# Kernel optimization log

Measured on AMD Instinct MI355X. Metric: run time of the kernel, lower is better.

The kernel has to match this reference:

```python
import jax, jax.numpy as jnp
import numpy as np

EMB = 1024
HEADS = 16
HEAD_DIM = EMB // HEADS
FF = 4 * EMB
EPS = 1e-5


def setup_inputs() -> dict:
    key = jax.random.key(0)
    ks = jax.random.split(key, 16)
    s = 0.02
    return {
        "x": jax.random.normal(ks[0], (2, 2048, EMB), dtype=jnp.float32),
        "ln1_g": jnp.ones((EMB,), jnp.float32),
        "ln1_b": jnp.zeros((EMB,), jnp.float32),
        "Wq": jax.random.normal(ks[1], (EMB, EMB), jnp.float32) * s,
        "bq": jnp.zeros((EMB,), jnp.float32),
        "Wk": jax.random.normal(ks[2], (EMB, EMB), jnp.float32) * s,
        "bk": jnp.zeros((EMB,), jnp.float32),
        "Wv": jax.random.normal(ks[3], (EMB, EMB), jnp.float32) * s,
        "bv": jnp.zeros((EMB,), jnp.float32),
        "Wo": jax.random.normal(ks[4], (EMB, EMB), jnp.float32) * s,
        "bo": jnp.zeros((EMB,), jnp.float32),
        "ln2_g": jnp.ones((EMB,), jnp.float32),
        "ln2_b": jnp.zeros((EMB,), jnp.float32),
        "W1": jax.random.normal(ks[5], (EMB, FF), jnp.float32) * s,
        "b1": jnp.zeros((FF,), jnp.float32),
        "W2": jax.random.normal(ks[6], (FF, EMB), jnp.float32) * s,
        "b2": jnp.zeros((EMB,), jnp.float32),
    }


def _layernorm(x, g, b):
    mu = jnp.mean(x, axis=-1, keepdims=True)
    var = jnp.var(x, axis=-1, keepdims=True)
    return (x - mu) * jax.lax.rsqrt(var + EPS) * g + b


def _attention(x, Wq, bq, Wk, bk, Wv, bv, Wo, bo):
    B, T, C = x.shape
    # [B,T,C] -> [B,H,T,Dh]
    def split(y):
        return y.reshape(B, T, HEADS, HEAD_DIM).transpose(0, 2, 1, 3)
    Q = split(x @ Wq + bq)
    K = split(x @ Wk + bk)
    V = split(x @ Wv + bv)
    att = jnp.einsum("bhqd,bhkd->bhqk", Q, K) / np.sqrt(HEAD_DIM).astype(np.float32)
    causal = jnp.tril(jnp.ones((T, T), bool))
    att = jnp.where(causal, att, -jnp.inf)
    att = jax.nn.softmax(att, axis=-1)
    out = jnp.einsum("bhqk,bhkd->bhqd", att, V)
    out = out.transpose(0, 2, 1, 3).reshape(B, T, C)
    return out @ Wo + bo


def reference(x, ln1_g, ln1_b, Wq, bq, Wk, bk, Wv, bv, Wo, bo,
              ln2_g, ln2_b, W1, b1, W2, b2):
    # dropout is identity in eval mode
    x = x + _attention(_layernorm(x, ln1_g, ln1_b), Wq, bq, Wk, bk, Wv, bv, Wo, bo)
    h = _layernorm(x, ln2_g, ln2_b)
    h = jax.nn.gelu(h @ W1 + b1, approximate=False) @ W2 + b2
    return x + h
```

## Files before the change

### kernel.cpp

```cpp
#include <hip/hip_runtime.h>
#include <hip/hip_bf16.h>

typedef __attribute__((ext_vector_type(4))) float f32x4;
typedef __attribute__((ext_vector_type(8))) short bf16x8;
typedef unsigned int u32;
typedef unsigned short u16;

#define GASP __attribute__((address_space(1)))
#define LASP __attribute__((address_space(3)))

__device__ __forceinline__ u16 f2bf(float f) {
  u32 u = __float_as_uint(f);
  return (u16)((u + 0x7fffu + ((u >> 16) & 1u)) >> 16);
}

__device__ __forceinline__ u32 cvtpk(float lo, float hi) {
  u32 r;
  asm("v_cvt_pk_bf16_f32 %0, %1, %2" : "=v"(r) : "v"(lo), "v"(hi));
  return r;
}

__device__ __forceinline__ void gl_lds16(const void* g, void* l) {
  __builtin_amdgcn_global_load_lds((const GASP u32*)g, (LASP u32*)l, 16, 0, 0);
}

struct CastArgs {
  const float* s[6];
  u16* d[6];
};

__global__ __launch_bounds__(256) void cast_w(CastArgs a) {
  int bid = blockIdx.x;
  int w, t, K, N, kshift;
  if (bid < 4096)      { w = bid >> 10; t = bid & 1023; K = 1024; N = 1024; kshift = 5; }
  else if (bid < 8192) { w = 4; t = bid - 4096; K = 1024; N = 4096; kshift = 5; }
  else                 { w = 5; t = bid - 8192; K = 4096; N = 1024; kshift = 7; }
  int tk = t & ((1 << kshift) - 1);
  int tn = t >> kshift;
  int k0 = tk << 5, n0 = tn << 5;
  const float* src = a.s[w];
  u16* dst = a.d[w];
  __shared__ u16 tile[32][36];
  int r = threadIdx.x >> 3, c0 = (threadIdx.x & 7) << 2;
  float4 v = *(const float4*)&src[(size_t)(k0 + r) * N + n0 + c0];
  tile[c0 + 0][r] = f2bf(v.x);
  tile[c0 + 1][r] = f2bf(v.y);
  tile[c0 + 2][r] = f2bf(v.z);
  tile[c0 + 3][r] = f2bf(v.w);
  __syncthreads();
  ushort4 o;
  o.x = tile[r][c0 + 0];
  o.y = tile[r][c0 + 1];
  o.z = tile[r][c0 + 2];
  o.w = tile[r][c0 + 3];
  *(ushort4*)&dst[(size_t)(n0 + r) * K + k0 + c0] = o;
}

__global__ __launch_bounds__(256) void ln_k(const float* __restrict__ x, const float* __restrict__ g,
                                            const float* __restrict__ b, u16* __restrict__ out) {
  int row = blockIdx.x;
  int tid = threadIdx.x;
  float4 v = *(const float4*)&x[(size_t)row * 1024 + tid * 4];
  float s = v.x + v.y + v.z + v.w;
  float ss = v.x * v.x + v.y * v.y + v.z * v.z + v.w * v.w;
#pragma unroll
  for (int o = 32; o >= 1; o >>= 1) {
    s += __shfl_xor(s, o, 64);
    ss += __shfl_xor(ss, o, 64);
  }
  __shared__ float red[8];
  int wv = tid >> 6;
  if ((tid & 63) == 0) { red[wv] = s; red[wv + 4] = ss; }
  __syncthreads();
  s = red[0] + red[1] + red[2] + red[3];
  ss = red[4] + red[5] + red[6] + red[7];
  float mu = s * (1.0f / 1024.0f);
  float var = ss * (1.0f / 1024.0f) - mu * mu;
  float rstd = rsqrtf(var + 1e-5f);
  float4 gv = *(const float4*)&g[tid * 4];
  float4 bv = *(const float4*)&b[tid * 4];
  ushort4 o4;
  o4.x = f2bf((v.x - mu) * rstd * gv.x + bv.x);
  o4.y = f2bf((v.y - mu) * rstd * gv.y + bv.y);
  o4.z = f2bf((v.z - mu) * rstd * gv.z + bv.z);
  o4.w = f2bf((v.w - mu) * rstd * gv.w + bv.w);
  *(ushort4*)&out[(size_t)row * 1024 + tid * 4] = o4;
}

template <int MODE>
__global__ __launch_bounds__(512, 2) void gemm_256(
    const u16* __restrict__ A, const u16* __restrict__ Bt,
    const float* __restrict__ bias0, const float* __restrict__ bias1, const float* __restrict__ bias2,
    void* outp, int rm, int rn, int xn, int M, int N, int K) {
  __shared__ __align__(16) u16 As[4][128 * 64];
  __shared__ __align__(16) u16 Bs[4][128 * 64];
  char* asB = (char*)As;
  char* bsB = (char*)Bs;
  const int tid = threadIdx.x;
  const int w = tid >> 6, lane = tid & 63;
  const int xcd = blockIdx.x & 7, idx = blockIdx.x >> 3;
  const int mt = (xcd / xn) * rm + (idx % rm);
  const int nt = (xcd % xn) * rn + (idx / rm);
  const int m0 = mt << 8, n0 = nt << 8;

  const int rA = tid >> 3;
  const int csw = ((tid & 7) ^ (rA & 7)) * 8;
  const u16* pA = A + (size_t)(m0 + rA) * K + csw;
  const u16* pB = Bt + (size_t)(n0 + rA) * K + csw;
  const int dstOff = tid * 16;

#define STG_A(kt, h, d_) do {                                            \
    const u16* s_ = pA + (size_t)((h) * 128) * K + (size_t)(kt) * 64;    \
    char* l_ = asB + ((d_) * 2 + (h)) * 16384 + dstOff;                  \
    gl_lds16(s_, l_);                                                    \
    gl_lds16(s_ + (size_t)64 * K, l_ + 8192);                            \
  } while (0)
#define STG_B(kt, h, d_) do {                                            \
    const u16* s_ = pB + (size_t)((h) * 128) * K + (size_t)(kt) * 64;    \
    char* l_ = bsB + ((d_) * 2 + (h)) * 16384 + dstOff;                  \
    gl_lds16(s_, l_);                                                    \
    gl_lds16(s_ + (size_t)64 * K, l_ + 8192);                            \
  } while (0)

  const int wr = w >> 2, wc = w & 3;
  const int g = lane >> 4, qi = lane & 15;

  int aOff[8][2], bOff[4][2];
#pragma unroll
  for (int mm = 0; mm < 8; ++mm) {
    int row = mm * 16 + qi;
#pragma unroll
    for (int ks = 0; ks < 2; ++ks)
      aOff[mm][ks] = row * 128 + (((ks * 4 + g) ^ (qi & 7)) << 4);
  }
#pragma unroll
  for (int nn = 0; nn < 4; ++nn) {
    int rowb = (wc & 1) * 64 + nn * 16 + qi;
#pragma unroll
    for (int ks = 0; ks < 2; ++ks)
      bOff[nn][ks] = rowb * 128 + (((ks * 4 + g) ^ (qi & 7)) << 4);
  }

  f32x4 acc[8][4];
#pragma unroll
  for (int i = 0; i < 8; ++i)
#pragma unroll
    for (int j = 0; j < 4; ++j) acc[i][j] = f32x4{0.f, 0.f, 0.f, 0.f};

#define MFMA16(MB, A00, A01, A10, A11) do {                                              \
    __builtin_amdgcn_s_setprio(1);                                                       \
    acc[(MB)][0] = __builtin_amdgcn_mfma_f32_16x16x32_bf16(A00, bv[0][0], acc[(MB)][0], 0, 0, 0); \
    acc[(MB)][1] = __builtin_amdgcn_mfma_f32_16x16x32_bf16(A00, bv[1][0], acc[(MB)][1], 0, 0, 0); \
    acc[(MB)][2] = __builtin_amdgcn_mfma_f32_16x16x32_bf16(A00, bv[2][0], acc[(MB)][2], 0, 0, 0); \
    acc[(MB)][3] = __builtin_amdgcn_mfma_f32_16x16x32_bf16(A00, bv[3][0], acc[(MB)][3], 0, 0, 0); \
    acc[(MB) + 1][0] = __builtin_amdgcn_mfma_f32_16x16x32_bf16(A10, bv[0][0], acc[(MB) + 1][0], 0, 0, 0); \
    acc[(MB) + 1][1] = __builtin_amdgcn_mfma_f32_16x16x32_bf16(A10, bv[1][0], acc[(MB) + 1][1], 0, 0, 0); \
    acc[(MB) + 1][2] = __builtin_amdgcn_mfma_f32_16x16x32_bf16(A10, bv[2][0], acc[(MB) + 1][2], 0, 0, 0); \
    acc[(MB) + 1][3] = __builtin_amdgcn_mfma_f32_16x16x32_bf16(A10, bv[3][0], acc[(MB) + 1][3], 0, 0, 0); \
    acc[(MB)][0] = __builtin_amdgcn_mfma_f32_16x16x32_bf16(A01, bv[0][1], acc[(MB)][0], 0, 0, 0); \
    acc[(MB)][1] = __builtin_amdgcn_mfma_f32_16x16x32_bf16(A01, bv[1][1], acc[(MB)][1], 0, 0, 0); \
    acc[(MB)][2] = __builtin_amdgcn_mfma_f32_16x16x32_bf16(A01, bv[2][1], acc[(MB)][2], 0, 0, 0); \
    acc[(MB)][3] = __builtin_amdgcn_mfma_f32_16x16x32_bf16(A01, bv[3][1], acc[(MB)][3], 0, 0, 0); \
    acc[(MB) + 1][0] = __builtin_amdgcn_mfma_f32_16x16x32_bf16(A11, bv[0][1], acc[(MB) + 1][0], 0, 0, 0); \
    acc[(MB) + 1][1] = __builtin_amdgcn_mfma_f32_16x16x32_bf16(A11, bv[1][1], acc[(MB) + 1][1], 0, 0, 0); \
    acc[(MB) + 1][2] = __builtin_amdgcn_mfma_f32_16x16x32_bf16(A11, bv[2][1], acc[(MB) + 1][2], 0, 0, 0); \
    acc[(MB) + 1][3] = __builtin_amdgcn_mfma_f32_16x16x32_bf16(A11, bv[3][1], acc[(MB) + 1][3], 0, 0, 0); \
    __builtin_amdgcn_s_setprio(0);                                                       \
  } while (0)

#define RDA(dst0, dst1, MB)                                          \
    bf16x8 dst0##0 = *(const bf16x8*)(asB + aTB + aOff[(MB)][0]);     \
    bf16x8 dst0##1 = *(const bf16x8*)(asB + aTB + aOff[(MB)][1]);     \
    bf16x8 dst1##0 = *(const bf16x8*)(asB + aTB + aOff[(MB) + 1][0]); \
    bf16x8 dst1##1 = *(const bf16x8*)(asB + aTB + aOff[(MB) + 1][1]);

  const int T = K >> 6;
  STG_A(0, 0, 0); STG_A(0, 1, 0);
  STG_B(0, 0, 0); STG_B(0, 1, 0);
  if (T > 1) {
    STG_B(1, 0, 1); STG_B(1, 1, 1);
    asm volatile("s_waitcnt vmcnt(4)" ::: "memory");
  } else {
    asm volatile("s_waitcnt vmcnt(0)" ::: "memory");
  }
  __builtin_amdgcn_s_barrier();

  for (int t = 0; t < T; ++t) {
    const int d = t & 1;
    const int aTB = (d * 2 + wr) * 16384;
    const int bTB = (d * 2 + (wc >> 1)) * 16384;
    bf16x8 bv[4][2];
#pragma unroll
    for (int nn = 0; nn < 4; ++nn) {
      bv[nn][0] = *(const bf16x8*)(bsB + bTB + bOff[nn][0]);
      bv[nn][1] = *(const bf16x8*)(bsB + bTB + bOff[nn][1]);
    }
    RDA(p0a, p0b, 0);
    asm volatile("" ::: "memory");
    if (t + 1 < T) STG_A(t + 1, 0, d ^ 1);
    __builtin_amdgcn_s_barrier();
    MFMA16(0, p0a0, p0a1, p0b0, p0b1);
    __builtin_amdgcn_s_barrier();
    {
      RDA(p1a, p1b, 2);
      asm volatile("" ::: "memory");
      if (t + 1 < T) STG_A(t + 1, 1, d ^ 1);
      __builtin_amdgcn_s_barrier();
      MFMA16(2, p1a0, p1a1, p1b0, p1b1);
      __builtin_amdgcn_s_barrier();
    }
    {
      RDA(p2a, p2b, 4);
      asm volatile("" ::: "memory");
      if (t + 2 < T) STG_B(t + 2, 0, d);
      __builtin_amdgcn_s_barrier();
      MFMA16(4, p2a0, p2a1, p2b0, p2b1);
      __builtin_amdgcn_s_barrier();
    }
    {
      RDA(p3a, p3b, 6);
      asm volatile("" ::: "memory");
      if (t + 2 < T) STG_B(t + 2, 1, d);
      __builtin_amdgcn_s_barrier();
      MFMA16(6, p3a0, p3a1, p3b0, p3b1);
      if (t < T - 2)       { asm volatile("s_waitcnt vmcnt(4)" ::: "memory"); }
      else if (t == T - 2) { asm volatile("s_waitcnt vmcnt(0)" ::: "memory"); }
      __builtin_amdgcn_s_barrier();
    }
  }
#undef MFMA16
#undef RDA
#undef STG_A
#undef STG_B

  const int ci = lane & 15;
#pragma unroll
  for (int mm = 0; mm < 8; ++mm) {
#pragma unroll
    for (int nn = 0; nn < 4; ++nn) {
      int colb = n0 + wc * 64 + nn * 16 + ci;
      int rowbase = m0 + wr * 128 + mm * 16 + 4 * g;
      f32x4 c = acc[mm][nn];
      if constexpr (MODE == 2) {
        int sel = colb >> 10;
        int cc = colb & 1023;
        const float* bp = sel == 0 ? bias0 : (sel == 1 ? bias1 : bias2);
        float bb = bp[cc];
        int h = cc >> 6, dd = cc & 63;
        int b_ = rowbase >> 11, tt = rowbase & 2047;
        if (sel == 2) {
          u16* op = (u16*)outp + 2ull * (4096ull * 1024ull);
          ushort4 o4;
          o4.x = f2bf(c[0] + bb);
          o4.y = f2bf(c[1] + bb);
          o4.z = f2bf(c[2] + bb);
          o4.w = f2bf(c[3] + bb);
          *(ushort4*)&op[((size_t)(b_ * 16 + h) * 64 + dd) * 2048 + tt] = o4;
        } else {
          float scale = (sel == 0) ? 0.125f : 1.0f;
          u16* op = (u16*)outp + (size_t)sel * (4096ull * 1024ull);
#pragma unroll
          for (int r = 0; r < 4; ++r)
            op[((size_t)(b_ * 16 + h) * 2048 + tt + r) * 64 + dd] = f2bf((c[r] + bb) * scale);
        }
      } else {
        float bb = bias0[colb];
#pragma unroll
        for (int r = 0; r < 4; ++r) {
          float v = c[r] + bb;
          float gl = 0.5f * v * (1.0f + erff(v * 0.70710678118654752f));
          ((u16*)outp)[(size_t)(rowbase + r) * N + colb] = f2bf(gl);
        }
      }
    }
  }
}

__global__ __launch_bounds__(512) void gemm_sk(
    const u16* __restrict__ A, const u16* __restrict__ Bt,
    const float* __restrict__ bias0, float* __restrict__ outp,
    const float* __restrict__ res, int M, int N, int K) {
  __shared__ __align__(16) union SM {
    struct { u16 As[2][4][128 * 32]; u16 Bs[2][4][128 * 32]; } t;
    float red[16][4][4][64];
  } sm;
  const int tid = threadIdx.x;
  const int w8 = tid >> 6, lane = tid & 63;
  const int gg = w8 >> 2, wl = w8 & 3;
  const int m0 = blockIdx.y << 7, n0 = blockIdx.x << 7;

  char* asB = (char*)sm.t.As[gg];
  char* bsB = (char*)sm.t.Bs[gg];
  const u16* aS[2];
  const u16* bS[2];
#pragma unroll
  for (int i = 0; i < 2; ++i) {
    int p = wl * 2048 + i * 1024 + lane * 16;
    int r = p >> 6;
    int cl = ((p >> 4) & 3) ^ ((r >> 1) & 3);
    aS[i] = A + (size_t)(m0 + r) * K + gg * 32 + cl * 8;
    bS[i] = Bt + (size_t)(n0 + r) * K + gg * 32 + cl * 8;
  }
  f32x4 acc[4][4];
#pragma unroll
  for (int i = 0; i < 4; ++i)
#pragma unroll
    for (int j = 0; j < 4; ++j) acc[i][j] = f32x4{0.f, 0.f, 0.f, 0.f};

  const int wr = wl >> 1, wc = wl & 1;
  int aOff[4], bOff[4];
#pragma unroll
  for (int mm = 0; mm < 4; ++mm) {
    int rowa = wr * 64 + mm * 16 + (lane & 15);
    aOff[mm] = rowa * 64 + (((lane >> 4) ^ ((rowa >> 1) & 3)) << 4);
    int rowb = wc * 64 + mm * 16 + (lane & 15);
    bOff[mm] = rowb * 64 + (((lane >> 4) ^ ((rowb >> 1) & 3)) << 4);
  }

  gl_lds16(aS[0], asB + wl * 2048);
  gl_lds16(aS[1], asB + wl * 2048 + 1024);
  gl_lds16(bS[0], bsB + wl * 2048);
  gl_lds16(bS[1], bsB + wl * 2048 + 1024);
  if (K > 64) {
    gl_lds16(aS[0] + 64, asB + 8192 + wl * 2048);
    gl_lds16(aS[1] + 64, asB + 8192 + wl * 2048 + 1024);
    gl_lds16(bS[0] + 64, bsB + 8192 + wl * 2048);
    gl_lds16(bS[1] + 64, bsB + 8192 + wl * 2048 + 1024);
  }
  if (K > 128) {
    gl_lds16(aS[0] + 128, asB + 16384 + wl * 2048);
    gl_lds16(aS[1] + 128, asB + 16384 + wl * 2048 + 1024);
    gl_lds16(bS[0] + 128, bsB + 16384 + wl * 2048);
    gl_lds16(bS[1] + 128, bsB + 16384 + wl * 2048 + 1024);
  }
  int buf = 0;
  for (int ks = 0; ks < K; ks += 64) {
    const int rem = ((K - ks) >> 6) - 1;
    if (rem >= 2)      { asm volatile("s_waitcnt vmcnt(8)" ::: "memory"); }
    else if (rem == 1) { asm volatile("s_waitcnt vmcnt(4)" ::: "memory"); }
    else               { asm volatile("s_waitcnt vmcnt(0)" ::: "memory"); }
    __builtin_amdgcn_s_barrier();
    asm volatile("" ::: "memory");
    if (ks + 192 < K) {
      const int nb = ((buf + 3) & 3) * 8192;
      gl_lds16(aS[0] + ks + 192, asB + nb + wl * 2048);
      gl_lds16(aS[1] + ks + 192, asB + nb + wl * 2048 + 1024);
      gl_lds16(bS[0] + ks + 192, bsB + nb + wl * 2048);
      gl_lds16(bS[1] + ks + 192, bsB + nb + wl * 2048 + 1024);
    }
    const int tb = buf * 8192;
    bf16x8 av[4], bv[4];
#pragma unroll
    for (int mm = 0; mm < 4; ++mm) av[mm] = *(const bf16x8*)(asB + tb + aOff[mm]);
#pragma unroll
    for (int nn = 0; nn < 4; ++nn) bv[nn] = *(const bf16x8*)(bsB + tb + bOff[nn]);
#pragma unroll
    for (int mm = 0; mm < 4; ++mm)
#pragma unroll
      for (int nn = 0; nn < 4; ++nn)
        acc[mm][nn] = __builtin_amdgcn_mfma_f32_16x16x32_bf16(av[mm], bv[nn], acc[mm][nn], 0, 0, 0);
    buf = (buf + 1) & 3;
  }

  __syncthreads();
  if (gg == 1) {
#pragma unroll
    for (int mm = 0; mm < 4; ++mm)
#pragma unroll
      for (int nn = 0; nn < 4; ++nn)
#pragma unroll
        for (int r = 0; r < 4; ++r) sm.red[mm * 4 + nn][r][wl][lane] = acc[mm][nn][r];
  }
  __syncthreads();
  if (gg == 0) {
    const int g = lane >> 4, ci = lane & 15;
#pragma unroll
    for (int mm = 0; mm < 4; ++mm) {
#pragma unroll
      for (int nn = 0; nn < 4; ++nn) {
        int colb = n0 + wc * 64 + nn * 16 + ci;
        int rowbase = m0 + wr * 64 + mm * 16 + 4 * g;
        float bb = bias0[colb];
#pragma unroll
        for (int r = 0; r < 4; ++r) {
          size_t idx = (size_t)(rowbase + r) * N + colb;
          outp[idx] = acc[mm][nn][r] + sm.red[mm * 4 + nn][r][wl][lane] + bb + res[idx];
        }
      }
    }
  }
}

__global__ __launch_bounds__(512) void attn_k(const u16* __restrict__ Q, const u16* __restrict__ Kg,
                                              const u16* __restrict__ Vt, u16* __restrict__ O) {
  __shared__ __align__(16) u16 Ks[2][64 * 64];
  __shared__ __align__(16) u16 Vs[2][64 * 64];
  const int bx = blockIdx.y;
  const int bh = blockIdx.x;
  const int tid = threadIdx.x, w = tid >> 6, lane = tid & 63;
  const int g = lane >> 4, qi = lane & 15;
  const u16* Qb = Q + (size_t)bh * 2048 * 64;
  const u16* Kb = Kg + (size_t)bh * 2048 * 64;
  const u16* Vtb = Vt + (size_t)bh * 64 * 2048;

  const int rS = tid >> 3, cS = tid & 7;
  const int csw = (cS ^ (rS & 7)) * 8;
  const u16* srcK = Kb + (size_t)rS * 64 + csw;
  const u16* srcV = Vtb + (size_t)rS * 2048 + csw;
  char* ksB = (char*)Ks;
  char* vsB = (char*)Vs;
  const int dstOff = tid * 16;

  int koff[4][2], voff[4][2];
#pragma unroll
  for (int t = 0; t < 4; ++t) {
    int row = 16 * t + qi;
#pragma unroll
    for (int h = 0; h < 2; ++h) koff[t][h] = row * 128 + (((4 * h + g) ^ (qi & 7)) << 4);
#pragma unroll
    for (int kt = 0; kt < 2; ++kt) voff[t][kt] = row * 128 + (((4 * kt + g) ^ (qi & 7)) << 4);
  }

  const int b_ = bh >> 4, hh = bh & 15;
  u32* Ou = (u32*)O;

  for (int job = 0; job < 2; ++job) {
    const int qt = job ? bx : 15 - bx;
    const int qmin = qt * 128 + w * 16;
    const int qrow = qmin + qi;
    const int qmaxw = qmin + 15;

    bf16x8 qf[2];
#pragma unroll
    for (int h = 0; h < 2; ++h)
      qf[h] = *(const bf16x8*)(Qb + (size_t)qrow * 64 + h * 32 + g * 8);

    f32x4 acc[4];
#pragma unroll
    for (int dt = 0; dt < 4; ++dt) acc[dt] = f32x4{0.f, 0.f, 0.f, 0.f};
    float m = -1e30f, lsum = 0.0f;

    __syncthreads();
    gl_lds16(srcK, ksB + dstOff);
    gl_lds16(srcV, vsB + dstOff);

    const int nsteps = 2 * qt + 2;
    int buf = 0;
    for (int s = 0; s < nsteps; ++s) {
      __syncthreads();
      if (s + 1 < nsteps) {
        int nb = buf ^ 1;
        gl_lds16(srcK + (size_t)(s + 1) * 4096, ksB + nb * 8192 + dstOff);
        gl_lds16(srcV + (size_t)(s + 1) * 64, vsB + nb * 8192 + dstOff);
      }
      const int kv0 = s * 64;
      if (kv0 <= qmaxw) {
        const int tb = buf * 8192;
        f32x4 st[4];
        __builtin_amdgcn_s_setprio(1);
#pragma unroll
        for (int t = 0; t < 4; ++t) {
          st[t] = f32x4{0.f, 0.f, 0.f, 0.f};
#pragma unroll
          for (int h = 0; h < 2; ++h) {
            bf16x8 kf = *(const bf16x8*)(ksB + tb + koff[t][h]);
            st[t] = __builtin_amdgcn_mfma_f32_16x16x32_bf16(kf, qf[h], st[t], 0, 0, 0);
          }
        }
        __builtin_amdgcn_s_setprio(0);
        float pvv[4][4];
        float tmax = -1e30f;
        if (kv0 + 63 > qmin) {
#pragma unroll
          for (int t = 0; t < 4; ++t)
#pragma unroll
            for (int r = 0; r < 4; ++r) {
              int key = kv0 + 16 * t + 4 * g + r;
              float sv = st[t][r];
              sv = (key <= qrow) ? sv : -1e30f;
              pvv[t][r] = sv;
              tmax = fmaxf(tmax, sv);
            }
        } else {
#pragma unroll
          for (int t = 0; t < 4; ++t)
#pragma unroll
            for (int r = 0; r < 4; ++r) {
              float sv = st[t][r];
              pvv[t][r] = sv;
              tmax = fmaxf(tmax, sv);
            }
        }
        tmax = fmaxf(tmax, __shfl_xor(tmax, 16, 64));
        tmax = fmaxf(tmax, __shfl_xor(tmax, 32, 64));
        if (!__all(tmax <= m + 8.0f)) {
          float mn = fmaxf(m, tmax);
          float corr = __expf(m - mn);
          lsum *= corr;
#pragma unroll
          for (int dt = 0; dt < 4; ++dt)
#pragma unroll
            for (int r = 0; r < 4; ++r) acc[dt][r] *= corr;
          m = mn;
        }
        float tsum = 0.f;
#pragma unroll
        for (int t = 0; t < 4; ++t)
#pragma unroll
          for (int r = 0; r < 4; ++r) {
            float e = __expf(pvv[t][r] - m);
            pvv[t][r] = e;
            tsum += e;
          }
        tsum += __shfl_xor(tsum, 16, 64);
        tsum += __shfl_xor(tsum, 32, 64);
        lsum += tsum;
        u32 pk[4][2], ex[4][2];
#pragma unroll
        for (int t = 0; t < 4; ++t)
#pragma unroll
          for (int p = 0; p < 2; ++p) {
            u32 v = cvtpk(pvv[t][2 * p], pvv[t][2 * p + 1]);
            pk[t][p] = v;
            ex[t][p] = (u32)__shfl_xor((int)v, 16, 64);
          }
        const bool ge = (g & 1) == 0;
        const bool G0 = (g >> 1) == 0;
        const bool innr = (g == 0) || (g == 3);
        u32 mm_[4][4];
#pragma unroll
        for (int t = 0; t < 4; ++t) {
          mm_[t][0] = ge ? pk[t][0] : ex[t][0];
          mm_[t][1] = ge ? pk[t][1] : ex[t][1];
          mm_[t][2] = ge ? ex[t][0] : pk[t][0];
          mm_[t][3] = ge ? ex[t][1] : pk[t][1];
        }
        union Frag { u32 u[4]; bf16x8 v; } f0, f1;
#pragma unroll
        for (int i = 0; i < 4; ++i) {
          u32 sel0 = G0 ? mm_[1][i] : mm_[0][i];
          u32 sel1 = G0 ? mm_[3][i] : mm_[2][i];
          u32 sw0 = (u32)__shfl_xor((int)sel0, 32, 64);
          u32 sw1 = (u32)__shfl_xor((int)sel1, 32, 64);
          u32 own0 = G0 ? mm_[0][i] : mm_[1][i];
          u32 own1 = G0 ? mm_[2][i] : mm_[3][i];
          f0.u[i] = innr ? own0 : sw0;
          f1.u[i] = innr ? own1 : sw1;
        }
        __builtin_amdgcn_s_setprio(1);
#pragma unroll
        for (int dt = 0; dt < 4; ++dt) {
          bf16x8 vfa = *(const bf16x8*)(vsB + tb + voff[dt][0]);
          acc[dt] = __builtin_amdgcn_mfma_f32_16x16x32_bf16(vfa, f0.v, acc[dt], 0, 0, 0);
          bf16x8 vfb = *(const bf16x8*)(vsB + tb + voff[dt][1]);
          acc[dt] = __builtin_amdgcn_mfma_f32_16x16x32_bf16(vfb, f1.v, acc[dt], 0, 0, 0);
        }
        __builtin_amdgcn_s_setprio(0);
      }
      buf ^= 1;
    }

    float rl = 1.0f / lsum;
    size_t rowq = (size_t)(b_ * 2048 + qrow);
#pragma unroll
    for (int dt = 0; dt < 4; ++dt) {
#pragma unroll
      for (int rp = 0; rp < 2; ++rp) {
        u16 lo = f2bf(acc[dt][rp * 2] * rl);
        u16 hi = f2bf(acc[dt][rp * 2 + 1] * rl);
        u32 pkd = (u32)lo | ((u32)hi << 16);
        size_t off = rowq * 1024 + hh * 64 + dt * 16 + 4 * g + rp * 2;
        Ou[off >> 1] = pkd;
      }
    }
  }
}

extern "C" void kernel_launch(void* const* d_in, const int* in_sizes, int n_in,
                              void* d_out, int out_size, void* d_ws, size_t ws_size,
                              hipStream_t stream) {
  const float* x    = (const float*)d_in[0];
  const float* ln1g = (const float*)d_in[1];
  const float* ln1b = (const float*)d_in[2];
  const float* Wq   = (const float*)d_in[3];
  const float* bq   = (const float*)d_in[4];
  const float* Wk   = (const float*)d_in[5];
  const float* bk   = (const float*)d_in[6];
  const float* Wv   = (const float*)d_in[7];
  const float* bv   = (const float*)d_in[8];
  const float* Wo   = (const float*)d_in[9];
  const float* bo   = (const float*)d_in[10];
  const float* ln2g = (const float*)d_in[11];
  const float* ln2b = (const float*)d_in[12];
  const float* W1   = (const float*)d_in[13];
  const float* b1   = (const float*)d_in[14];
  const float* W2   = (const float*)d_in[15];
  const float* b2   = (const float*)d_in[16];

  char* ws = (char*)d_ws;
  const size_t MB = 1ull << 20;
  u16* WqT = (u16*)(ws + 0 * MB);
  u16* WkT = (u16*)(ws + 2 * MB);
  u16* WvT = (u16*)(ws + 4 * MB);
  u16* WoT = (u16*)(ws + 6 * MB);
  u16* W1T = (u16*)(ws + 8 * MB);
  u16* W2T = (u16*)(ws + 16 * MB);
  u16* XN  = (u16*)(ws + 24 * MB);
  u16* Qb  = (u16*)(ws + 32 * MB);
  u16* Kb  = (u16*)(ws + 40 * MB);
  u16* Vtb = (u16*)(ws + 48 * MB);
  u16* Ob  = (u16*)(ws + 56 * MB);
  u16* Gb  = (u16*)(ws + 32 * MB);

  CastArgs ca;
  ca.s[0] = Wq; ca.s[1] = Wk; ca.s[2] = Wv; ca.s[3] = Wo; ca.s[4] = W1; ca.s[5] = W2;
  ca.d[0] = WqT; ca.d[1] = WkT; ca.d[2] = WvT; ca.d[3] = WoT; ca.d[4] = W1T; ca.d[5] = W2T;
  cast_w<<<12288, 256, 0, stream>>>(ca);

  ln_k<<<4096, 256, 0, stream>>>(x, ln1g, ln1b, XN);

  gemm_256<2><<<192, 512, 0, stream>>>(XN, WqT, bq, bk, bv, Qb, 4, 6, 2, 4096, 3072, 1024);

  attn_k<<<dim3(32, 8), 512, 0, stream>>>(Qb, Kb, Vtb, Ob);

  gemm_sk<<<dim3(8, 32), 512, 0, stream>>>(Ob, WoT, bo, (float*)d_out, x, 4096, 1024, 1024);

  ln_k<<<4096, 256, 0, stream>>>((const float*)d_out, ln2g, ln2b, XN);

  gemm_256<3><<<256, 512, 0, stream>>>(XN, W1T, b1, nullptr, nullptr, Gb, 8, 4, 4, 4096, 4096, 1024);

  gemm_sk<<<dim3(8, 32), 512, 0, stream>>>(Gb, W2T, b2, (float*)d_out, (const float*)d_out, 4096, 1024, 4096);
}
```

Measured before the change: 239.2 us.

## Load K/V fragments directly from global memory instead of LDS double buffering

The attention kernel drops the shared-memory double-buffered K/V staging and its block-wide barriers. Each wave now loads its own K and V^T MFMA fragments straight from global memory and iterates only up to its own causal limit. This removes the __syncthreads and LDS traffic, but each of the 8 waves in a block re-reads the same K/V tiles from global/L2, and load latency is no longer hidden by prefetching.

```diff
diff --git a/kernel.cpp b/kernel.cpp
--- a/kernel.cpp
+++ b/kernel.cpp
@@ -393,8 +393,6 @@
 
 __global__ __launch_bounds__(512) void attn_k(const u16* __restrict__ Q, const u16* __restrict__ Kg,
                                               const u16* __restrict__ Vt, u16* __restrict__ O) {
-  __shared__ __align__(16) u16 Ks[2][64 * 64];
-  __shared__ __align__(16) u16 Vs[2][64 * 64];
   const int bx = blockIdx.y;
   const int bh = blockIdx.x;
   const int tid = threadIdx.x, w = tid >> 6, lane = tid & 63;
@@ -403,24 +401,6 @@
   const u16* Kb = Kg + (size_t)bh * 2048 * 64;
   const u16* Vtb = Vt + (size_t)bh * 64 * 2048;
 
-  const int rS = tid >> 3, cS = tid & 7;
-  const int csw = (cS ^ (rS & 7)) * 8;
-  const u16* srcK = Kb + (size_t)rS * 64 + csw;
-  const u16* srcV = Vtb + (size_t)rS * 2048 + csw;
-  char* ksB = (char*)Ks;
-  char* vsB = (char*)Vs;
-  const int dstOff = tid * 16;
-
-  int koff[4][2], voff[4][2];
-#pragma unroll
-  for (int t = 0; t < 4; ++t) {
-    int row = 16 * t + qi;
-#pragma unroll
-    for (int h = 0; h < 2; ++h) koff[t][h] = row * 128 + (((4 * h + g) ^ (qi & 7)) << 4);
-#pragma unroll
-    for (int kt = 0; kt < 2; ++kt) voff[t][kt] = row * 128 + (((4 * kt + g) ^ (qi & 7)) << 4);
-  }
-
   const int b_ = bh >> 4, hh = bh & 15;
   u32* Ou = (u32*)O;
 
@@ -428,7 +408,6 @@
     const int qt = job ? bx : 15 - bx;
     const int qmin = qt * 128 + w * 16;
     const int qrow = qmin + qi;
-    const int qmaxw = qmin + 15;
 
     bf16x8 qf[2];
 #pragma unroll
@@ -440,124 +419,119 @@
     for (int dt = 0; dt < 4; ++dt) acc[dt] = f32x4{0.f, 0.f, 0.f, 0.f};
     float m = -1e30f, lsum = 0.0f;
 
-    __syncthreads();
-    gl_lds16(srcK, ksB + dstOff);
-    gl_lds16(srcV, vsB + dstOff);
-
-    const int nsteps = 2 * qt + 2;
-    int buf = 0;
-    for (int s = 0; s < nsteps; ++s) {
-      __syncthreads();
-      if (s + 1 < nsteps) {
-        int nb = buf ^ 1;
-        gl_lds16(srcK + (size_t)(s + 1) * 4096, ksB + nb * 8192 + dstOff);
-        gl_lds16(srcV + (size_t)(s + 1) * 64, vsB + nb * 8192 + dstOff);
-      }
+    const int smax = qmin >> 6;
+    for (int s = 0; s <= smax; ++s) {
       const int kv0 = s * 64;
-      if (kv0 <= qmaxw) {
-        const int tb = buf * 8192;
-        f32x4 st[4];
-        __builtin_amdgcn_s_setprio(1);
-#pragma unroll
-        for (int t = 0; t < 4; ++t) {
-          st[t] = f32x4{0.f, 0.f, 0.f, 0.f};
-#pragma unroll
-          for (int h = 0; h < 2; ++h) {
-            bf16x8 kf = *(const bf16x8*)(ksB + tb + koff[t][h]);
-            st[t] = __builtin_amdgcn_mfma_f32_16x16x32_bf16(kf, qf[h], st[t], 0, 0, 0);
+      const u16* kb = Kb + (size_t)kv0 * 64;
+      const u16* vb = Vtb + kv0;
+      bf16x8 kf0[4], kf1[4], vfa[4], vfb[4];
+#pragma unroll
+      for (int t = 0; t < 4; ++t) {
+        const u16* kr = kb + (size_t)(16 * t + qi) * 64;
+        kf0[t] = *(const bf16x8*)(kr + g * 8);
+        kf1[t] = *(const bf16x8*)(kr + 32 + g * 8);
+      }
+#pragma unroll
+      for (int dt = 0; dt < 4; ++dt) {
+        const u16* vr = vb + (size_t)(16 * dt + qi) * 2048;
+        vfa[dt] = *(const bf16x8*)(vr + g * 8);
+        vfb[dt] = *(const bf16x8*)(vr + 32 + g * 8);
+      }
+      f32x4 st[4];
+      __builtin_amdgcn_s_setprio(1);
+#pragma unroll
+      for (int t = 0; t < 4; ++t) {
+        st[t] = f32x4{0.f, 0.f, 0.f, 0.f};
+        st[t] = __builtin_amdgcn_mfma_f32_16x16x32_bf16(kf0[t], qf[0], st[t], 0, 0, 0);
+        st[t] = __builtin_amdgcn_mfma_f32_16x16x32_bf16(kf1[t], qf[1], st[t], 0, 0, 0);
+      }
+      __builtin_amdgcn_s_setprio(0);
+      float pvv[4][4];
+      float tmax = -1e30f;
+      if (kv0 + 63 > qmin) {
+#pragma unroll
+        for (int t = 0; t < 4; ++t)
+#pragma unroll
+          for (int r = 0; r < 4; ++r) {
+            int key = kv0 + 16 * t + 4 * g + r;
+            float sv = st[t][r];
+            sv = (key <= qrow) ? sv : -1e30f;
+            pvv[t][r] = sv;
+            tmax = fmaxf(tmax, sv);
           }
+      } else {
+#pragma unroll
+        for (int t = 0; t < 4; ++t)
+#pragma unroll
+          for (int r = 0; r < 4; ++r) {
+            float sv = st[t][r];
+            pvv[t][r] = sv;
+            tmax = fmaxf(tmax, sv);
+          }
+      }
+      tmax = fmaxf(tmax, __shfl_xor(tmax, 16, 64));
+      tmax = fmaxf(tmax, __shfl_xor(tmax, 32, 64));
+      if (!__all(tmax <= m + 8.0f)) {
+        float mn = fmaxf(m, tmax);
+        float corr = __expf(m - mn);
+        lsum *= corr;
+#pragma unroll
+        for (int dt = 0; dt < 4; ++dt)
+#pragma unroll
+          for (int r = 0; r < 4; ++r) acc[dt][r] *= corr;
+        m = mn;
+      }
+      float tsum = 0.f;
+#pragma unroll
+      for (int t = 0; t < 4; ++t)
+#pragma unroll
+        for (int r = 0; r < 4; ++r) {
+          float e = __expf(pvv[t][r] - m);
+          pvv[t][r] = e;
+          tsum += e;
         }
-        __builtin_amdgcn_s_setprio(0);
-        float pvv[4][4];
-        float tmax = -1e30f;
-        if (kv0 + 63 > qmin) {
-#pragma unroll
-          for (int t = 0; t < 4; ++t)
-#pragma unroll
-            for (int r = 0; r < 4; ++r) {
-              int key = kv0 + 16 * t + 4 * g + r;
-              float sv = st[t][r];
-              sv = (key <= qrow) ? sv : -1e30f;
-              pvv[t][r] = sv;
-              tmax = fmaxf(tmax, sv);
-            }
-        } else {
-#pragma unroll
-          for (int t = 0; t < 4; ++t)
-#pragma unroll
-            for (int r = 0; r < 4; ++r) {
-              float sv = st[t][r];
-              pvv[t][r] = sv;
-              tmax = fmaxf(tmax, sv);
-            }
+      tsum += __shfl_xor(tsum, 16, 64);
+      tsum += __shfl_xor(tsum, 32, 64);
+      lsum += tsum;
+      u32 pk[4][2], ex[4][2];
+#pragma unroll
+      for (int t = 0; t < 4; ++t)
+#pragma unroll
+        for (int p = 0; p < 2; ++p) {
+          u32 v = cvtpk(pvv[t][2 * p], pvv[t][2 * p + 1]);
+          pk[t][p] = v;
+          ex[t][p] = (u32)__shfl_xor((int)v, 16, 64);
         }
-        tmax = fmaxf(tmax, __shfl_xor(tmax, 16, 64));
-        tmax = fmaxf(tmax, __shfl_xor(tmax, 32, 64));
-        if (!__all(tmax <= m + 8.0f)) {
-          float mn = fmaxf(m, tmax);
-          float corr = __expf(m - mn);
-          lsum *= corr;
-#pragma unroll
-          for (int dt = 0; dt < 4; ++dt)
-#pragma unroll
-            for (int r = 0; r < 4; ++r) acc[dt][r] *= corr;
-          m = mn;
-        }
-        float tsum = 0.f;
-#pragma unroll
-        for (int t = 0; t < 4; ++t)
-#pragma unroll
-          for (int r = 0; r < 4; ++r) {
-            float e = __expf(pvv[t][r] - m);
-            pvv[t][r] = e;
-            tsum += e;
-          }
-        tsum += __shfl_xor(tsum, 16, 64);
-        tsum += __shfl_xor(tsum, 32, 64);
-        lsum += tsum;
-        u32 pk[4][2], ex[4][2];
-#pragma unroll
-        for (int t = 0; t < 4; ++t)
-#pragma unroll
-          for (int p = 0; p < 2; ++p) {
-            u32 v = cvtpk(pvv[t][2 * p], pvv[t][2 * p + 1]);
-            pk[t][p] = v;
-            ex[t][p] = (u32)__shfl_xor((int)v, 16, 64);
-          }
-        const bool ge = (g & 1) == 0;
-        const bool G0 = (g >> 1) == 0;
-        const bool innr = (g == 0) || (g == 3);
-        u32 mm_[4][4];
-#pragma unroll
-        for (int t = 0; t < 4; ++t) {
-          mm_[t][0] = ge ? pk[t][0] : ex[t][0];
-          mm_[t][1] = ge ? pk[t][1] : ex[t][1];
-          mm_[t][2] = ge ? ex[t][0] : pk[t][0];
-          mm_[t][3] = ge ? ex[t][1] : pk[t][1];
-        }
-        union Frag { u32 u[4]; bf16x8 v; } f0, f1;
-#pragma unroll
-        for (int i = 0; i < 4; ++i) {
-          u32 sel0 = G0 ? mm_[1][i] : mm_[0][i];
-          u32 sel1 = G0 ? mm_[3][i] : mm_[2][i];
-          u32 sw0 = (u32)__shfl_xor((int)sel0, 32, 64);
-          u32 sw1 = (u32)__shfl_xor((int)sel1, 32, 64);
-          u32 own0 = G0 ? mm_[0][i] : mm_[1][i];
-          u32 own1 = G0 ? mm_[2][i] : mm_[3][i];
-          f0.u[i] = innr ? own0 : sw0;
-          f1.u[i] = innr ? own1 : sw1;
-        }
-        __builtin_amdgcn_s_setprio(1);
-#pragma unroll
-        for (int dt = 0; dt < 4; ++dt) {
-          bf16x8 vfa = *(const bf16x8*)(vsB + tb + voff[dt][0]);
-          acc[dt] = __builtin_amdgcn_mfma_f32_16x16x32_bf16(vfa, f0.v, acc[dt], 0, 0, 0);
-          bf16x8 vfb = *(const bf16x8*)(vsB + tb + voff[dt][1]);
-          acc[dt] = __builtin_amdgcn_mfma_f32_16x16x32_bf16(vfb, f1.v, acc[dt], 0, 0, 0);
-        }
-        __builtin_amdgcn_s_setprio(0);
-      }
-      buf ^= 1;
+      const bool ge = (g & 1) == 0;
+      const bool G0 = (g >> 1) == 0;
+      const bool innr = (g == 0) || (g == 3);
+      u32 mm_[4][4];
+#pragma unroll
+      for (int t = 0; t < 4; ++t) {
+        mm_[t][0] = ge ? pk[t][0] : ex[t][0];
+        mm_[t][1] = ge ? pk[t][1] : ex[t][1];
+        mm_[t][2] = ge ? ex[t][0] : pk[t][0];
+        mm_[t][3] = ge ? ex[t][1] : pk[t][1];
+      }
+      union Frag { u32 u[4]; bf16x8 v; } f0, f1;
+#pragma unroll
+      for (int i = 0; i < 4; ++i) {
+        u32 sel0 = G0 ? mm_[1][i] : mm_[0][i];
+        u32 sel1 = G0 ? mm_[3][i] : mm_[2][i];
+        u32 sw0 = (u32)__shfl_xor((int)sel0, 32, 64);
+        u32 sw1 = (u32)__shfl_xor((int)sel1, 32, 64);
+        u32 own0 = G0 ? mm_[0][i] : mm_[1][i];
+        u32 own1 = G0 ? mm_[2][i] : mm_[3][i];
+        f0.u[i] = innr ? own0 : sw0;
+        f1.u[i] = innr ? own1 : sw1;
+      }
+      __builtin_amdgcn_s_setprio(1);
+#pragma unroll
+      for (int dt = 0; dt < 4; ++dt) {
+        acc[dt] = __builtin_amdgcn_mfma_f32_16x16x32_bf16(vfa[dt], f0.v, acc[dt], 0, 0, 0);
+        acc[dt] = __builtin_amdgcn_mfma_f32_16x16x32_bf16(vfb[dt], f1.v, acc[dt], 0, 0, 0);
+      }
+      __builtin_amdgcn_s_setprio(0);
     }
 
     float rl = 1.0f / lsum;
```

After: 302.1 us. 26.3% more time.
